# Performance work log

Measured on AMD Instinct MI355X. Metric: run time of the kernel, lower is better.

Reference implementation:

```python
import jax, jax.numpy as jnp
import numpy as np

D_MODEL, N_QUERY, N_HEAD = 1024, 2, 8
D_HEAD = D_MODEL // (N_QUERY * N_HEAD)  # 64
KV = D_HEAD * N_HEAD                    # 512


def setup_inputs() -> dict:
    key = jax.random.key(0)
    ks = jax.random.split(key, 6)
    B, S = 2, 2048
    x = jax.random.normal(ks[0], (B, S, D_MODEL), jnp.float32)
    Wq = jax.random.normal(ks[1], (D_MODEL, D_MODEL), jnp.float32) / np.sqrt(D_MODEL)
    Wk = jax.random.normal(ks[2], (D_MODEL, KV), jnp.float32) / np.sqrt(D_MODEL)
    Wv = jax.random.normal(ks[3], (D_MODEL, KV), jnp.float32) / np.sqrt(D_MODEL)
    memory = jax.random.normal(ks[4], (KV, KV), jnp.float32)
    memory_norm = jnp.ones((KV,), jnp.float32)
    memory_weight = jnp.ones((1,), jnp.float32)
    return {"x": x, "Wq": Wq, "Wk": Wk, "Wv": Wv,
            "memory": memory, "memory_norm": memory_norm,
            "memory_weight": memory_weight}


def reference(x, Wq, Wk, Wv, memory, memory_norm, memory_weight):
    B, S, _ = x.shape
    QH = N_QUERY * N_HEAD
    scale = 1.0 / jnp.sqrt(jnp.float32(D_HEAD))

    q = x @ Wq          # (B,S,D_MODEL)
    k = x @ Wk          # (B,S,KV)
    v = x @ Wv          # (B,S,KV)

    # --- Eq. 6: grouped scaled dot-product attention ---
    q4 = q.reshape(B, S, QH, D_HEAD)                    # flat query split
    k4 = jnp.repeat(k.reshape(B, S, N_HEAD, D_HEAD), N_QUERY, axis=2)  # (B,S,QH,D)
    v4 = jnp.repeat(v.reshape(B, S, N_HEAD, D_HEAD), N_QUERY, axis=2)
    scores = jnp.einsum('bsnd,btnd->bnst', q4, k4) * scale  # (B,QH,S,S)
    probs = jax.nn.softmax(scores, axis=-1)
    a_dot = jnp.einsum('bnst,btnd->bsnd', probs, v4)        # (B,S,QH,D)

    # --- Eq. 7: memory read (grouped over n_query, width n_head*d_head) ---
    sigma_q = jax.nn.elu(q.reshape(B, S, N_QUERY, KV))      # (B,S,Q,KV)
    num = sigma_q @ memory                                   # (B,S,Q,KV)
    den = (sigma_q @ memory_norm)[..., None]                 # (B,S,Q,1)
    a_mem = (num / den).reshape(B, S, QH, D_HEAD)

    # --- Eq. 8/9: memory update (delta rule) ---
    sigma_k = jax.nn.elu(k)                                  # (B,S,KV)
    retrieved = (sigma_k @ memory) / (sigma_k @ memory_norm)[..., None]
    new_memory = memory + jnp.einsum('bsk,bsv->kv', sigma_k, v - retrieved)
    new_memory_norm = memory_norm + jnp.sum(sigma_k, axis=(0, 1))

    # --- Eq. 10: sigmoid-gated fusion ---
    w = jax.nn.sigmoid(memory_weight)                        # (1,)
    out = (a_dot * (1.0 - w) + a_mem * w).reshape(B, S, D_MODEL)
    return out, new_memory, new_memory_norm
```

## Files before the change

kernel.cpp:

```cpp
#include <hip/hip_runtime.h>
#include <hip/hip_bf16.h>

#define BB 2
#define SS 2048
#define DM 1024
#define KVD 512
#define NH 8
#define NQ 2
#define QH 16
#define DH 64
#define MROWS 4096

typedef float f32x4 __attribute__((ext_vector_type(4)));
typedef short short8 __attribute__((ext_vector_type(8)));
typedef short short4v __attribute__((ext_vector_type(4)));
typedef unsigned uint2v __attribute__((ext_vector_type(2)));

__device__ __forceinline__ float elu_f(float x) {
    return x > 0.0f ? x : (__expf(x) - 1.0f);
}

__device__ __forceinline__ short f2bf(float f) {
    union { float f; unsigned u; } v; v.f = f;
    unsigned r = v.u + 0x7FFFu + ((v.u >> 16) & 1u);
    return (short)(r >> 16);
}
__device__ __forceinline__ float bf2f(short s) {
    union { unsigned u; float f; } v;
    v.u = ((unsigned)(unsigned short)s) << 16;
    return v.f;
}
__device__ __forceinline__ unsigned cvtpk(float lo, float hi) {
    unsigned u;
    asm("v_cvt_pk_bf16_f32 %0, %1, %2" : "=v"(u) : "v"(lo), "v"(hi));
    return u;
}

__device__ __forceinline__ int swzs(int row, int byteoff) {
    return (row * 128 + (byteoff ^ ((row & 7) << 4))) >> 1;
}

#define GLD16(gp, lp) __builtin_amdgcn_global_load_lds( \
    (const __attribute__((address_space(1))) void*)(gp), \
    (__attribute__((address_space(3))) void*)(lp), 16, 0, 0)

__device__ __forceinline__ void stage_gl(const short* __restrict__ src, int ld,
                                         int row0, int k0, short* L,
                                         int wv, int lane) {
    const int srow = lane >> 3, sslot = lane & 7;
    #pragma unroll
    for (int i = 0; i < 4; i++) {
        int row = wv * 32 + i * 8 + srow;
        int slot = sslot ^ (row & 7);
        GLD16(&src[(size_t)(row0 + row) * ld + k0 + slot * 8],
              &L[(wv * 32 + i * 8) * 64]);
    }
}

__device__ __forceinline__ void stage_gl64(const short* __restrict__ src, int ld,
                                           int row0, int k0, short* L,
                                           int wv, int lane) {
    const int srow = lane >> 3, sslot = lane & 7;
    #pragma unroll
    for (int i = 0; i < 2; i++) {
        int row = wv * 16 + i * 8 + srow;
        int slot = sslot ^ (row & 7);
        GLD16(&src[(size_t)(row0 + row) * ld + k0 + slot * 8],
              &L[(wv * 16 + i * 8) * 64]);
    }
}

__device__ __forceinline__ void mma_tile(const short* __restrict__ Als,
                                         const short* __restrict__ Bls,
                                         int mb, int nb, int qr, int kg,
                                         f32x4 acc[4][4]) {
    #pragma unroll
    for (int kc = 0; kc < 2; kc++) {
        short8 af[4], bg[4];
        #pragma unroll
        for (int mi = 0; mi < 4; mi++)
            af[mi] = *(const short8*)&Als[swzs(mb + mi * 16 + qr, kc * 64 + kg * 16)];
        #pragma unroll
        for (int ni = 0; ni < 4; ni++)
            bg[ni] = *(const short8*)&Bls[swzs(nb + ni * 16 + qr, kc * 64 + kg * 16)];
        #pragma unroll
        for (int mi = 0; mi < 4; mi++)
            #pragma unroll
            for (int ni = 0; ni < 4; ni++)
                acc[mi][ni] = __builtin_amdgcn_mfma_f32_16x16x32_bf16(
                    af[mi], bg[ni], acc[mi][ni], 0, 0, 0);
    }
}

__device__ __forceinline__ void mma_tile64(const short* __restrict__ Als,
                                           const short* __restrict__ Bls,
                                           int mb, int nb, int qr, int kg,
                                           f32x4 acc[2][2]) {
    #pragma unroll
    for (int kc = 0; kc < 2; kc++) {
        short8 af[2], bg[2];
        #pragma unroll
        for (int mi = 0; mi < 2; mi++)
            af[mi] = *(const short8*)&Als[swzs(mb + mi * 16 + qr, kc * 64 + kg * 16)];
        #pragma unroll
        for (int ni = 0; ni < 2; ni++)
            bg[ni] = *(const short8*)&Bls[swzs(nb + ni * 16 + qr, kc * 64 + kg * 16)];
        #pragma unroll
        for (int mi = 0; mi < 2; mi++)
            #pragma unroll
            for (int ni = 0; ni < 2; ni++)
                acc[mi][ni] = __builtin_amdgcn_mfma_f32_16x16x32_bf16(
                    af[mi], bg[ni], acc[mi][ni], 0, 0, 0);
    }
}

__global__ __launch_bounds__(256) void prep_all(
        const float* __restrict__ x, const float* __restrict__ Wq,
        const float* __restrict__ Wk, const float* __restrict__ Wv,
        const float* __restrict__ memory,
        short* __restrict__ xb, short* __restrict__ wtb,
        short* __restrict__ memtb) {
    __shared__ float Ts[64][65];
    const int blk = blockIdx.x;
    const int tid = threadIdx.x;

    if (blk < 2048) {
        int i = (blk * 256 + tid) * 8;
        float4 a = *(const float4*)&x[i];
        float4 b = *(const float4*)&x[i + 4];
        short8 s;
        s[0] = f2bf(a.x); s[1] = f2bf(a.y); s[2] = f2bf(a.z); s[3] = f2bf(a.w);
        s[4] = f2bf(b.x); s[5] = f2bf(b.y); s[6] = f2bf(b.z); s[7] = f2bf(b.w);
        *(short8*)&xb[i] = s;
        return;
    }
    if (blk < 2560) {
        int idx = blk - 2048;
        const int k0 = (idx & 15) * 64, n0 = (idx >> 4) * 64;
        const float* W; int ld, c0;
        if (n0 < 1024)      { W = Wq; ld = 1024; c0 = n0; }
        else if (n0 < 1536) { W = Wk; ld = 512;  c0 = n0 - 1024; }
        else                { W = Wv; ld = 512;  c0 = n0 - 1536; }
        #pragma unroll
        for (int i = 0; i < 16; i++) {
            int e = tid + 256 * i;
            int kk = e >> 6, nn = e & 63;
            Ts[nn][kk] = W[(size_t)(k0 + kk) * ld + c0 + nn];
        }
        __syncthreads();
        #pragma unroll
        for (int i = 0; i < 16; i++) {
            int e = tid + 256 * i;
            int nn = e >> 6, kk = e & 63;
            wtb[(size_t)(n0 + nn) * 1024 + k0 + kk] = f2bf(Ts[nn][kk]);
        }
        return;
    }
    {
        int idx = blk - 2560;
        const int k0 = (idx & 7) * 64, n0 = (idx >> 3) * 64;
        #pragma unroll
        for (int i = 0; i < 16; i++) {
            int e = tid + 256 * i;
            int kk = e >> 6, nn = e & 63;
            Ts[nn][kk] = memory[(size_t)(k0 + kk) * 512 + n0 + nn];
        }
        __syncthreads();
        #pragma unroll
        for (int i = 0; i < 16; i++) {
            int e = tid + 256 * i;
            int nn = e >> 6, kk = e & 63;
            memtb[(size_t)(n0 + nn) * 512 + k0 + kk] = f2bf(Ts[nn][kk]);
        }
    }
}

__global__ __launch_bounds__(256) void gemm_qkv_mfma(
        const short* __restrict__ xb, const short* __restrict__ wtb,
        short* __restrict__ q, short* __restrict__ k, short* __restrict__ v,
        short* __restrict__ qelu, short* __restrict__ kelu,
        short* __restrict__ keluT, short* __restrict__ vt) {
    __shared__ __align__(16) short SMEM[16640];
    short* Als = SMEM;
    short* Bls = SMEM + 8192;
    short (*Tls)[130] = (short(*)[130])SMEM;
    const int n0 = blockIdx.x * 128, m0 = blockIdx.y * 128;
    const int tid = threadIdx.x, lane = tid & 63, wv = tid >> 6;
    const int qr = lane & 15, kg = lane >> 4;
    const int mb = (wv >> 1) * 64, nb = (wv & 1) * 64;

    f32x4 acc[4][4];
    #pragma unroll
    for (int i = 0; i < 4; i++)
        #pragma unroll
        for (int j = 0; j < 4; j++) acc[i][j] = (f32x4){0.f, 0.f, 0.f, 0.f};

    for (int kt = 0; kt < 16; kt++) {
        stage_gl(xb, 1024, m0, kt * 64, Als, wv, lane);
        stage_gl(wtb, 1024, n0, kt * 64, Bls, wv, lane);
        __syncthreads();
        mma_tile(Als, Bls, mb, nb, qr, kg, acc);
        __syncthreads();
    }

    const int kind = (n0 < 1024) ? 0 : (n0 < 1536) ? 1 : 2;
    #pragma unroll
    for (int mi = 0; mi < 4; mi++)
        #pragma unroll
        for (int ni = 0; ni < 4; ni++)
            #pragma unroll
            for (int r = 0; r < 4; r++) {
                int lr = mb + mi * 16 + kg * 4 + r;
                int lc = nb + ni * 16 + qr;
                int gr = m0 + lr;
                short val = f2bf(acc[mi][ni][r]);
                if (kind == 0) {
                    int gc = n0 + lc;
                    q[(size_t)gr * 1024 + gc] = val;
                    qelu[(size_t)gr * 1024 + gc] = f2bf(elu_f(bf2f(val)));
                } else if (kind == 1) {
                    int gc = (n0 - 1024) + lc;
                    k[(size_t)gr * 512 + gc] = val;
                    short ev = f2bf(elu_f(bf2f(val)));
                    kelu[(size_t)gr * 512 + gc] = ev;
                    Tls[lr][lc] = ev;
                } else {
                    int gc = (n0 - 1536) + lc;
                    v[(size_t)gr * 512 + gc] = val;
                    Tls[lr][lc] = val;
                }
            }

    if (kind == 0) return;
    __syncthreads();
    const int lane16 = tid & 15, rgrp = tid >> 4;
    #pragma unroll
    for (int p = 0; p < 8; p++) {
        int lc2 = p * 16 + rgrp;
        short8 s;
        #pragma unroll
        for (int e = 0; e < 8; e++) s[e] = Tls[lane16 * 8 + e][lc2];
        if (kind == 1) {
            int gcT = (n0 - 1024) + lc2;
            *(short8*)&keluT[(size_t)gcT * 4096 + m0 + lane16 * 8] = s;
        } else {
            int gc = (n0 - 1536) + lc2;
            int bh2 = (m0 >> 11) * 8 + (gc >> 6);
            *(short8*)&vt[((size_t)bh2 * 64 + (gc & 63)) * SS + (m0 & 2047)
                          + lane16 * 8] = s;
        }
    }
}

__global__ __launch_bounds__(256) void den_colsum(
        const short* __restrict__ qelu, const short* __restrict__ kelu,
        const short* __restrict__ keluT, const float* __restrict__ norm,
        float* __restrict__ den_q, float* __restrict__ den_k,
        float* __restrict__ out_norm) {
    const int wavei = threadIdx.x >> 6, lane = threadIdx.x & 63;
    const int blk = blockIdx.x;
    if (blk < 3072) {
        const int row = blk * 4 + wavei;
        const short* src; float* den;
        if (row < 8192) { src = qelu + (size_t)row * 512; den = den_q + row; }
        else { int rk = row - 8192; src = kelu + (size_t)rk * 512; den = den_k + rk; }
        short8 vv = *(const short8*)&src[lane * 8];
        float4 n0 = *(const float4*)&norm[lane * 8];
        float4 n1 = *(const float4*)&norm[lane * 8 + 4];
        float nn[8] = {n0.x, n0.y, n0.z, n0.w, n1.x, n1.y, n1.z, n1.w};
        float s = 0.0f;
        #pragma unroll
        for (int j = 0; j < 8; j++) s += bf2f(vv[j]) * nn[j];
        #pragma unroll
        for (int off = 32; off >= 1; off >>= 1) s += __shfl_xor(s, off);
        if (lane == 0) *den = s;
    } else {
        const int row = (blk - 3072) * 4 + wavei;
        float s = 0.0f;
        #pragma unroll
        for (int j = 0; j < 8; j++) {
            short8 vv = *(const short8*)&keluT[(size_t)row * 4096 + j * 512 + lane * 8];
            #pragma unroll
            for (int e = 0; e < 8; e++) s += bf2f(vv[e]);
        }
        #pragma unroll
        for (int off = 32; off >= 1; off >>= 1) s += __shfl_xor(s, off);
        if (lane == 0) out_norm[row] = norm[row] + s;
    }
}

__global__ __launch_bounds__(256) void gemm_amem_mfma(
        const short* __restrict__ qelu, const short* __restrict__ memtb,
        const short* __restrict__ adotb, const float* __restrict__ den_q,
        const float* __restrict__ mw, float* __restrict__ out) {
    __shared__ __align__(16) short Als[4096];
    __shared__ __align__(16) short Bls[4096];
    const int n0 = blockIdx.x * 64, m0 = blockIdx.y * 64;
    const int tid = threadIdx.x, lane = tid & 63, wv = tid >> 6;
    const int qr = lane & 15, kg = lane >> 4;
    const int mb = (wv >> 1) * 32, nb = (wv & 1) * 32;
    const float wgt = 1.0f / (1.0f + __expf(-mw[0]));

    f32x4 acc[2][2];
    #pragma unroll
    for (int i = 0; i < 2; i++)
        #pragma unroll
        for (int j = 0; j < 2; j++) acc[i][j] = (f32x4){0.f, 0.f, 0.f, 0.f};

    for (int kt = 0; kt < 8; kt++) {
        stage_gl64(qelu, 512, m0, kt * 64, Als, wv, lane);
        stage_gl64(memtb, 512, n0, kt * 64, Bls, wv, lane);
        __syncthreads();
        mma_tile64(Als, Bls, mb, nb, qr, kg, acc);
        __syncthreads();
    }

    #pragma unroll
    for (int mi = 0; mi < 2; mi++) {
        int gr0 = m0 + mb + mi * 16 + kg * 4;
        float invd[4];
        #pragma unroll
        for (int r = 0; r < 4; r++) invd[r] = wgt / den_q[gr0 + r];
        #pragma unroll
        for (int ni = 0; ni < 2; ni++) {
            int gc = n0 + nb + ni * 16 + qr;
            #pragma unroll
            for (int r = 0; r < 4; r++) {
                size_t fo = (size_t)(gr0 + r) * 512 + gc;
                out[fo] = bf2f(adotb[fo]) * (1.0f - wgt)
                        + acc[mi][ni][r] * invd[r];
            }
        }
    }
}

__global__ __launch_bounds__(256) void gemm_u_mfma(
        const short* __restrict__ kelu, const short* __restrict__ memtb,
        const short* __restrict__ vb, const float* __restrict__ den_k,
        short* __restrict__ uT) {
    __shared__ __align__(16) short Als[4096];
    __shared__ __align__(16) short Bls[4096];
    const int n0 = blockIdx.x * 64, m0 = blockIdx.y * 64;
    const int tid = threadIdx.x, lane = tid & 63, wv = tid >> 6;
    const int qr = lane & 15, kg = lane >> 4;
    const int mb = (wv >> 1) * 32, nb = (wv & 1) * 32;

    f32x4 acc[2][2];
    #pragma unroll
    for (int i = 0; i < 2; i++)
        #pragma unroll
        for (int j = 0; j < 2; j++) acc[i][j] = (f32x4){0.f, 0.f, 0.f, 0.f};

    for (int kt = 0; kt < 8; kt++) {
        stage_gl64(kelu, 512, m0, kt * 64, Als, wv, lane);
        stage_gl64(memtb, 512, n0, kt * 64, Bls, wv, lane);
        __syncthreads();
        mma_tile64(Als, Bls, mb, nb, qr, kg, acc);
        __syncthreads();
    }

    #pragma unroll
    for (int mi = 0; mi < 2; mi++) {
        int gr0 = m0 + mb + mi * 16 + kg * 4;
        float invd[4];
        #pragma unroll
        for (int r = 0; r < 4; r++) invd[r] = 1.0f / den_k[gr0 + r];
        #pragma unroll
        for (int ni = 0; ni < 2; ni++) {
            int gc = n0 + nb + ni * 16 + qr;
            short4v st;
            #pragma unroll
            for (int r = 0; r < 4; r++)
                st[r] = f2bf(bf2f(vb[(size_t)(gr0 + r) * 512 + gc])
                             - acc[mi][ni][r] * invd[r]);
            *(short4v*)&uT[(size_t)gc * 4096 + gr0] = st;
        }
    }
}

__global__ __launch_bounds__(256) void gemm_delta_mfma(
        const short* __restrict__ keluT, const short* __restrict__ uT,
        float* __restrict__ dpart) {
    __shared__ __align__(16) short Als[4096];
    __shared__ __align__(16) short Bls[4096];
    const int j0 = blockIdx.x * 64, i0 = blockIdx.y * 64;
    const int kcz = blockIdx.z;
    const int tid = threadIdx.x, lane = tid & 63, wv = tid >> 6;
    const int qr = lane & 15, kg = lane >> 4;
    const int mb = (wv >> 1) * 32, nb = (wv & 1) * 32;

    f32x4 acc[2][2];
    #pragma unroll
    for (int i = 0; i < 2; i++)
        #pragma unroll
        for (int j = 0; j < 2; j++) acc[i][j] = (f32x4){0.f, 0.f, 0.f, 0.f};

    for (int kt = 0; kt < 4; kt++) {
        int k0 = kcz * 256 + kt * 64;
        stage_gl64(keluT, 4096, i0, k0, Als, wv, lane);
        stage_gl64(uT, 4096, j0, k0, Bls, wv, lane);
        __syncthreads();
        mma_tile64(Als, Bls, mb, nb, qr, kg, acc);
        __syncthreads();
    }

    #pragma unroll
    for (int mi = 0; mi < 2; mi++)
        #pragma unroll
        for (int ni = 0; ni < 2; ni++)
            #pragma unroll
            for (int r = 0; r < 4; r++) {
                int gr = i0 + mb + mi * 16 + kg * 4 + r;
                int gc = j0 + nb + ni * 16 + qr;
                dpart[(size_t)kcz * (KVD * KVD) + (size_t)gr * 512 + gc] = acc[mi][ni][r];
            }
}

__global__ __launch_bounds__(256) void delta_final(
        const float* __restrict__ part, const float* __restrict__ memory,
        float* __restrict__ out_mem) {
    const int idx = blockIdx.x * 256 + threadIdx.x;
    float s = memory[idx];
    #pragma unroll
    for (int kc = 0; kc < 16; kc++) s += part[(size_t)kc * (KVD * KVD) + idx];
    out_mem[idx] = s;
}

__global__ __launch_bounds__(256) void flash_attn_mfma(
        const short* __restrict__ qb, const short* __restrict__ kb,
        const short* __restrict__ vt, short* __restrict__ adotb) {
    __shared__ __align__(16) short Klds[2][4096];
    __shared__ __align__(16) short Vlds[2][4096];
    __shared__ __align__(16) short Plds[4096];

    const int id = blockIdx.x;
    const int low3 = id & 7, rest = id >> 3;
    const int xblk = rest & 31, bhhi = rest >> 5;
    const int bh = (bhhi << 3) | low3;
    const int r0 = xblk * 64;
    const int b = bh >> 4, qh = bh & 15;
    const int kvh = qh >> 1;
    const int tid = threadIdx.x;
    const int lane = tid & 63, wv = tid >> 6;
    const int qr = lane & 15, kg = lane >> 4;
    const float scale2 = 0.125f * 1.44269504f;

    const int srow = lane >> 3, sslot = lane & 7;

    const int krow0 = wv * 16 + srow, krow1 = krow0 + 8;
    const short* kp0 = kb + (size_t)(b * SS + krow0) * KVD + kvh * DH
                       + (sslot ^ (krow0 & 7)) * 8;
    const short* kp1 = kb + (size_t)(b * SS + krow1) * KVD + kvh * DH
                       + (sslot ^ (krow1 & 7)) * 8;
    const short* vp0 = vt + ((size_t)(b * NH + kvh) * DH + krow0) * SS
                       + (sslot ^ (krow0 & 7)) * 8;
    const short* vp1 = vt + ((size_t)(b * NH + kvh) * DH + krow1) * SS
                       + (sslot ^ (krow1 & 7)) * 8;

    short8 qa[2];
    {
        const short* qp = qb + (size_t)(b * SS + r0 + wv * 16 + qr) * DM + qh * DH;
        qa[0] = *(const short8*)&qp[kg * 8];
        qa[1] = *(const short8*)&qp[32 + kg * 8];
        #pragma unroll
        for (int e = 0; e < 8; e++) {
            qa[0][e] = f2bf(bf2f(qa[0][e]) * scale2);
            qa[1][e] = f2bf(bf2f(qa[1][e]) * scale2);
        }
    }
    short8 ones;
    #pragma unroll
    for (int e = 0; e < 8; e++) ones[e] = (short)0x3F80;

    f32x4 oacc[4];
    #pragma unroll
    for (int dt = 0; dt < 4; dt++) oacc[dt] = (f32x4){0.f, 0.f, 0.f, 0.f};
    f32x4 lacc = (f32x4){0.f, 0.f, 0.f, 0.f};

    short* Pw = Plds + wv * 1024;
    short* Kdst0 = &Klds[0][(wv * 16 + 0) * 64];
    short* Kdst1 = &Klds[0][(wv * 16 + 8) * 64];
    short* Vdst0 = &Vlds[0][(wv * 16 + 0) * 64];
    short* Vdst1 = &Vlds[0][(wv * 16 + 8) * 64];

    GLD16(kp0, Kdst0); GLD16(kp1, Kdst1);
    GLD16(vp0, Vdst0); GLD16(vp1, Vdst1);

    for (int it = 0; it < 32; ++it) {
        const int cur = it & 1;
        __syncthreads();
        if (it + 1 < 32) {
            kp0 += 64 * KVD; kp1 += 64 * KVD; vp0 += 64; vp1 += 64;
            int nb2 = (cur ^ 1) * 4096;
            GLD16(kp0, Kdst0 + nb2); GLD16(kp1, Kdst1 + nb2);
            GLD16(vp0, Vdst0 + nb2); GLD16(vp1, Vdst1 + nb2);
        }

        f32x4 sacc[4];
        #pragma unroll
        for (int j = 0; j < 4; j++) sacc[j] = (f32x4){0.f, 0.f, 0.f, 0.f};
        __builtin_amdgcn_s_setprio(1);
        #pragma unroll
        for (int c = 0; c < 2; c++) {
            #pragma unroll
            for (int j = 0; j < 4; j++) {
                short8 kf = *(const short8*)&Klds[cur][swzs(j * 16 + qr, kg * 16 + c * 64)];
                sacc[j] = __builtin_amdgcn_mfma_f32_16x16x32_bf16(kf, qa[c], sacc[j], 0, 0, 0);
            }
        }
        __builtin_amdgcn_s_setprio(0);

        #pragma unroll
        for (int j = 0; j < 4; j++) {
            float p0 = exp2f(sacc[j][0]);
            float p1 = exp2f(sacc[j][1]);
            float p2 = exp2f(sacc[j][2]);
            float p3 = exp2f(sacc[j][3]);
            uint2v u;
            u[0] = cvtpk(p0, p1);
            u[1] = cvtpk(p2, p3);
            *(uint2v*)&Pw[swzs(qr, j * 32 + kg * 8)] = u;
        }
        asm volatile("s_waitcnt lgkmcnt(0)" ::: "memory");
        __builtin_amdgcn_sched_barrier(0);

        __builtin_amdgcn_s_setprio(1);
        #pragma unroll
        for (int c = 0; c < 2; c++) {
            short8 pf = *(const short8*)&Pw[swzs(qr, kg * 16 + c * 64)];
            lacc = __builtin_amdgcn_mfma_f32_16x16x32_bf16(ones, pf, lacc, 0, 0, 0);
            #pragma unroll
            for (int dt = 0; dt < 4; dt++) {
                short8 vf = *(const short8*)&Vlds[cur][swzs(dt * 16 + qr, kg * 16 + c * 64)];
                oacc[dt] = __builtin_amdgcn_mfma_f32_16x16x32_bf16(vf, pf, oacc[dt], 0, 0, 0);
            }
        }
        __builtin_amdgcn_s_setprio(0);
    }

    float inv = 1.0f / lacc[0];
    short* ap = adotb + (size_t)(b * SS + r0 + wv * 16 + qr) * DM + qh * DH;
    #pragma unroll
    for (int dt = 0; dt < 4; dt++) {
        short4v st;
        #pragma unroll
        for (int r = 0; r < 4; r++) st[r] = f2bf(oacc[dt][r] * inv);
        *(short4v*)&ap[dt * 16 + kg * 4] = st;
    }
}

extern "C" void kernel_launch(void* const* d_in, const int* in_sizes, int n_in,
                              void* d_out, int out_size, void* d_ws, size_t ws_size,
                              hipStream_t stream) {
    const float* x      = (const float*)d_in[0];
    const float* Wq     = (const float*)d_in[1];
    const float* Wk     = (const float*)d_in[2];
    const float* Wv     = (const float*)d_in[3];
    const float* memory = (const float*)d_in[4];
    const float* mnorm  = (const float*)d_in[5];
    const float* mw     = (const float*)d_in[6];

    float* out_f   = (float*)d_out;
    float* out_mem = out_f + (size_t)MROWS * DM;
    float* out_nrm = out_mem + (size_t)KVD * KVD;

    short*  xb    = (short*)d_ws;
    short*  wtb   = xb + 4194304;
    short*  memtb = wtb + 2097152;
    short*  qb    = memtb + 262144;
    short*  kbuf  = qb + 4194304;
    short*  vbuf  = kbuf + 2097152;
    short*  vt    = vbuf + 2097152;
    short*  qelu  = vt + 2097152;
    short*  kelu  = qelu + 4194304;
    short*  keluT = kelu + 2097152;
    short*  uT    = keluT + 2097152;
    float*  den_q = (float*)(uT + 2097152);
    float*  den_k = den_q + 8192;
    short*  adotb = xb;
    float*  dpart = (float*)d_ws;

    prep_all<<<2624, 256, 0, stream>>>(x, Wq, Wk, Wv, memory, xb, wtb, memtb);

    gemm_qkv_mfma<<<dim3(16, 32), 256, 0, stream>>>(xb, wtb, qb, kbuf, vbuf,
                                                    qelu, kelu, keluT, vt);

    flash_attn_mfma<<<1024, 256, 0, stream>>>(qb, kbuf, vt, adotb);

    den_colsum<<<3200, 256, 0, stream>>>(qelu, kelu, keluT, mnorm,
                                         den_q, den_k, out_nrm);

    gemm_amem_mfma<<<dim3(8, 128), 256, 0, stream>>>(qelu, memtb, adotb,
                                                     den_q, mw, out_f);

    gemm_u_mfma<<<dim3(8, 64), 256, 0, stream>>>(kelu, memtb, vbuf, den_k, uT);
    gemm_delta_mfma<<<dim3(8, 8, 16), 256, 0, stream>>>(keluT, uT, dpart);
    delta_final<<<1024, 256, 0, stream>>>(dpart, memory, out_mem);
}
```

Baseline: 150.1 us.

## Double-buffer shared-memory tiles in the four MFMA GEMM kernels

Converts the QKV, a_mem, u and delta GEMM main loops to double-buffered LDS staging. The next K-tile is loaded into the alternate buffer while MFMAs run on the current one, which drops one barrier per iteration. This doubles LDS use per block (64 KB in the QKV kernel), which may lower occupancy. How much overlap is gained depends on whether stage_gl issues its loads asynchronously or serially.

```diff
diff --git a/kernel.cpp b/kernel.cpp
--- a/kernel.cpp
+++ b/kernel.cpp
@@ -180,9 +180,7 @@
         short* __restrict__ q, short* __restrict__ k, short* __restrict__ v,
         short* __restrict__ qelu, short* __restrict__ kelu,
         short* __restrict__ keluT, short* __restrict__ vt) {
-    __shared__ __align__(16) short SMEM[16640];
-    short* Als = SMEM;
-    short* Bls = SMEM + 8192;
+    __shared__ __align__(16) short SMEM[32768];
     short (*Tls)[130] = (short(*)[130])SMEM;
     const int n0 = blockIdx.x * 128, m0 = blockIdx.y * 128;
     const int tid = threadIdx.x, lane = tid & 63, wv = tid >> 6;
@@ -195,13 +193,22 @@
         #pragma unroll
         for (int j = 0; j < 4; j++) acc[i][j] = (f32x4){0.f, 0.f, 0.f, 0.f};
 
+    stage_gl(xb, 1024, m0, 0, SMEM, wv, lane);
+    stage_gl(wtb, 1024, n0, 0, SMEM + 8192, wv, lane);
+
     for (int kt = 0; kt < 16; kt++) {
-        stage_gl(xb, 1024, m0, kt * 64, Als, wv, lane);
-        stage_gl(wtb, 1024, n0, kt * 64, Bls, wv, lane);
+        const int cur = kt & 1;
+        short* Acur = SMEM + cur * 16384;
+        short* Bcur = Acur + 8192;
         __syncthreads();
-        mma_tile(Als, Bls, mb, nb, qr, kg, acc);
-        __syncthreads();
-    }
+        if (kt + 1 < 16) {
+            short* Anxt = SMEM + (cur ^ 1) * 16384;
+            stage_gl(xb, 1024, m0, (kt + 1) * 64, Anxt, wv, lane);
+            stage_gl(wtb, 1024, n0, (kt + 1) * 64, Anxt + 8192, wv, lane);
+        }
+        mma_tile(Acur, Bcur, mb, nb, qr, kg, acc);
+    }
+    __syncthreads();
 
     const int kind = (n0 < 1024) ? 0 : (n0 < 1536) ? 1 : 2;
     #pragma unroll
@@ -293,8 +300,7 @@
         const short* __restrict__ qelu, const short* __restrict__ memtb,
         const short* __restrict__ adotb, const float* __restrict__ den_q,
         const float* __restrict__ mw, float* __restrict__ out) {
-    __shared__ __align__(16) short Als[4096];
-    __shared__ __align__(16) short Bls[4096];
+    __shared__ __align__(16) short SMEM[16384];
     const int n0 = blockIdx.x * 64, m0 = blockIdx.y * 64;
     const int tid = threadIdx.x, lane = tid & 63, wv = tid >> 6;
     const int qr = lane & 15, kg = lane >> 4;
@@ -307,12 +313,19 @@
         #pragma unroll
         for (int j = 0; j < 2; j++) acc[i][j] = (f32x4){0.f, 0.f, 0.f, 0.f};
 
+    stage_gl64(qelu, 512, m0, 0, SMEM, wv, lane);
+    stage_gl64(memtb, 512, n0, 0, SMEM + 4096, wv, lane);
     for (int kt = 0; kt < 8; kt++) {
-        stage_gl64(qelu, 512, m0, kt * 64, Als, wv, lane);
-        stage_gl64(memtb, 512, n0, kt * 64, Bls, wv, lane);
+        const int cur = kt & 1;
+        short* Acur = SMEM + cur * 8192;
+        short* Bcur = Acur + 4096;
         __syncthreads();
-        mma_tile64(Als, Bls, mb, nb, qr, kg, acc);
-        __syncthreads();
+        if (kt + 1 < 8) {
+            short* Anxt = SMEM + (cur ^ 1) * 8192;
+            stage_gl64(qelu, 512, m0, (kt + 1) * 64, Anxt, wv, lane);
+            stage_gl64(memtb, 512, n0, (kt + 1) * 64, Anxt + 4096, wv, lane);
+        }
+        mma_tile64(Acur, Bcur, mb, nb, qr, kg, acc);
     }
 
     #pragma unroll
@@ -338,8 +351,7 @@
         const short* __restrict__ kelu, const short* __restrict__ memtb,
         const short* __restrict__ vb, const float* __restrict__ den_k,
         short* __restrict__ uT) {
-    __shared__ __align__(16) short Als[4096];
-    __shared__ __align__(16) short Bls[4096];
+    __shared__ __align__(16) short SMEM[16384];
     const int n0 = blockIdx.x * 64, m0 = blockIdx.y * 64;
     const int tid = threadIdx.x, lane = tid & 63, wv = tid >> 6;
     const int qr = lane & 15, kg = lane >> 4;
@@ -351,12 +363,19 @@
         #pragma unroll
         for (int j = 0; j < 2; j++) acc[i][j] = (f32x4){0.f, 0.f, 0.f, 0.f};
 
+    stage_gl64(kelu, 512, m0, 0, SMEM, wv, lane);
+    stage_gl64(memtb, 512, n0, 0, SMEM + 4096, wv, lane);
     for (int kt = 0; kt < 8; kt++) {
-        stage_gl64(kelu, 512, m0, kt * 64, Als, wv, lane);
-        stage_gl64(memtb, 512, n0, kt * 64, Bls, wv, lane);
+        const int cur = kt & 1;
+        short* Acur = SMEM + cur * 8192;
+        short* Bcur = Acur + 4096;
         __syncthreads();
-        mma_tile64(Als, Bls, mb, nb, qr, kg, acc);
-        __syncthreads();
+        if (kt + 1 < 8) {
+            short* Anxt = SMEM + (cur ^ 1) * 8192;
+            stage_gl64(kelu, 512, m0, (kt + 1) * 64, Anxt, wv, lane);
+            stage_gl64(memtb, 512, n0, (kt + 1) * 64, Anxt + 4096, wv, lane);
+        }
+        mma_tile64(Acur, Bcur, mb, nb, qr, kg, acc);
     }
 
     #pragma unroll
@@ -381,8 +400,7 @@
 __global__ __launch_bounds__(256) void gemm_delta_mfma(
         const short* __restrict__ keluT, const short* __restrict__ uT,
         float* __restrict__ dpart) {
-    __shared__ __align__(16) short Als[4096];
-    __shared__ __align__(16) short Bls[4096];
+    __shared__ __align__(16) short SMEM[16384];
     const int j0 = blockIdx.x * 64, i0 = blockIdx.y * 64;
     const int kcz = blockIdx.z;
     const int tid = threadIdx.x, lane = tid & 63, wv = tid >> 6;
@@ -395,13 +413,20 @@
         #pragma unroll
         for (int j = 0; j < 2; j++) acc[i][j] = (f32x4){0.f, 0.f, 0.f, 0.f};
 
+    stage_gl64(keluT, 4096, i0, kcz * 256, SMEM, wv, lane);
+    stage_gl64(uT, 4096, j0, kcz * 256, SMEM + 4096, wv, lane);
     for (int kt = 0; kt < 4; kt++) {
-        int k0 = kcz * 256 + kt * 64;
-        stage_gl64(keluT, 4096, i0, k0, Als, wv, lane);
-        stage_gl64(uT, 4096, j0, k0, Bls, wv, lane);
+        const int cur = kt & 1;
+        short* Acur = SMEM + cur * 8192;
+        short* Bcur = Acur + 4096;
         __syncthreads();
-        mma_tile64(Als, Bls, mb, nb, qr, kg, acc);
-        __syncthreads();
+        if (kt + 1 < 4) {
+            int k0 = kcz * 256 + (kt + 1) * 64;
+            short* Anxt = SMEM + (cur ^ 1) * 8192;
+            stage_gl64(keluT, 4096, i0, k0, Anxt, wv, lane);
+            stage_gl64(uT, 4096, j0, k0, Anxt + 4096, wv, lane);
+        }
+        mma_tile64(Acur, Bcur, mb, nb, qr, kg, acc);
     }
 
     #pragma unroll
```

Result: no change. 149.2 us (-0.6%).
